# Kernel optimization log

Measured on AMD Instinct MI355X. Metric: run time of the kernel, lower is better.

## Reference

```python
import jax, jax.numpy as jnp
import numpy as np

B, S, H, R = 32, 512, 1024, 64


def _bernoulli(key, shape, p=0.05):
    return (jax.random.uniform(key, shape) < p).astype(jnp.float32)


def setup_inputs() -> dict:
    key = jax.random.key(0)
    ks = jax.random.split(key, 16)
    context = jax.random.normal(ks[0], (B, S, H), dtype=jnp.float32)
    masks = jnp.ones((B, S), dtype=jnp.float32)
    all_subject_heads = _bernoulli(ks[1], (B, S))
    all_subject_tails = _bernoulli(ks[2], (B, S))
    # one-hot subject head/tail positions (tail >= head)
    h_pos = jax.random.randint(ks[3], (B,), 0, S // 2)
    t_pos = h_pos + jax.random.randint(ks[4], (B,), 0, 8)
    subject_head = jax.nn.one_hot(h_pos, S, dtype=jnp.float32)
    subject_tail = jax.nn.one_hot(t_pos, S, dtype=jnp.float32)
    object_heads = _bernoulli(ks[5], (B, S, R))
    object_tails = _bernoulli(ks[6], (B, S, R))
    # learned parameters (PyTorch Linear: y = x @ W.T + b; store as [in, out])
    sc = 1.0 / np.sqrt(H)
    Ws_h = jax.random.uniform(ks[7], (H, 1), minval=-sc, maxval=sc)
    bs_h = jnp.zeros((1,), dtype=jnp.float32)
    Ws_t = jax.random.uniform(ks[8], (H, 1), minval=-sc, maxval=sc)
    bs_t = jnp.zeros((1,), dtype=jnp.float32)
    Wo_h = jax.random.uniform(ks[9], (H, R), minval=-sc, maxval=sc)
    bo_h = jnp.zeros((R,), dtype=jnp.float32)
    Wo_t = jax.random.uniform(ks[10], (H, R), minval=-sc, maxval=sc)
    bo_t = jnp.zeros((R,), dtype=jnp.float32)
    return dict(context=context, masks=masks,
                all_subject_heads=all_subject_heads, all_subject_tails=all_subject_tails,
                subject_head=subject_head, subject_tail=subject_tail,
                object_heads=object_heads, object_tails=object_tails,
                Ws_h=Ws_h, bs_h=bs_h, Ws_t=Ws_t, bs_t=bs_t,
                Wo_h=Wo_h, bo_h=bo_h, Wo_t=Wo_t, bo_t=bo_t)


def _bce_with_logits(logits, targets):
    # numerically stable, matches F.binary_cross_entropy_with_logits(reduction='none')
    return jnp.maximum(logits, 0.0) - logits * targets + jnp.log1p(jnp.exp(-jnp.abs(logits)))


def _masked_loss(gold, pred, mask):
    loss = _bce_with_logits(pred, gold)
    if loss.ndim != mask.ndim:
        mask = mask[..., None]
    return jnp.sum(loss * mask) / jnp.sum(mask)


def reference(context, masks, all_subject_heads, all_subject_tails,
              subject_head, subject_tail, object_heads, object_tails,
              Ws_h, bs_h, Ws_t, bs_t, Wo_h, bo_h, Wo_t, bo_t):
    # subject logits: [B,S]
    pred_subject_heads = (context @ Ws_h + bs_h)[..., 0]
    pred_subject_tails = (context @ Ws_t + bs_t)[..., 0]
    # subject pooling: one-hot [B,S] x context [B,S,H] -> [B,H]
    sub_h = jnp.einsum('bs,bsh->bh', subject_head, context)
    sub_t = jnp.einsum('bs,bsh->bh', subject_tail, context)
    subject = (sub_h + sub_t) * 0.5
    context_subject = context + subject[:, None, :]  # [B,S,H]
    pred_object_heads = context_subject @ Wo_h + bo_h  # [B,S,R]
    pred_object_tails = context_subject @ Wo_t + bo_t  # [B,S,R]
    loss = (_masked_loss(all_subject_heads, pred_subject_heads, masks)
            + _masked_loss(all_subject_tails, pred_subject_tails, masks)
            + _masked_loss(object_heads, pred_object_heads, masks)
            + _masked_loss(object_tails, pred_object_tails, masks))
    return loss
```

## Files before the change

kernel.cpp:

```cpp
#include <hip/hip_runtime.h>


#define B_  32
#define S_  512
#define H_  1024
#define R_  64
#define M_  (B_ * S_)
#define NPAD 160
#define NVALID 130
#define MT 128
#define CGC 80
#define TBLK 20
#define NTHR 512
#define NKS (H_ / 32)

typedef __attribute__((ext_vector_type(4))) float  floatx4;
typedef __attribute__((ext_vector_type(8))) short  short8;
typedef __attribute__((ext_vector_type(8))) unsigned short u16x8;

__device__ __forceinline__ unsigned short f2bf(float f) {
    unsigned int u = __float_as_uint(f);
    u = (u + 0x7FFFu + ((u >> 16) & 1u)) >> 16;
    return (unsigned short)u;
}

__device__ __forceinline__ short8 cvt8(float4 a, float4 b) {
    union { unsigned short us[8]; short8 s8; } u;
    u.us[0] = f2bf(a.x); u.us[1] = f2bf(a.y); u.us[2] = f2bf(a.z); u.us[3] = f2bf(a.w);
    u.us[4] = f2bf(b.x); u.us[5] = f2bf(b.y); u.us[6] = f2bf(b.z); u.us[7] = f2bf(b.w);
    return u.s8;
}

__device__ __forceinline__ void gload16(const void* g, void* l) {
    __builtin_amdgcn_global_load_lds(
        (const __attribute__((address_space(1))) unsigned int*)g,
        (__attribute__((address_space(3))) unsigned int*)l, 16, 0, 0);
}

__global__ __launch_bounds__(256) void aux_kernel(
        const float* __restrict__ ctx, const float* __restrict__ head,
        const float* __restrict__ tail, const float* __restrict__ masks,
        const float* __restrict__ Wo_h, const float* __restrict__ Wo_t,
        const float* __restrict__ Ws_h, const float* __restrict__ Ws_t,
        const float* __restrict__ bo_h, const float* __restrict__ bo_t,
        const float* __restrict__ bs_h, const float* __restrict__ bs_t,
        unsigned short* __restrict__ WtG, float* __restrict__ rowBias,
        float* __restrict__ accum) {
    const int tid = threadIdx.x;
    __shared__ float tr[32][257];
    __shared__ float subj[H_];
    __shared__ float partS[4][256];
    __shared__ int cnt;
    __shared__ int   sidx[8];
    __shared__ float sw[8];

    if (blockIdx.x < TBLK) {
        const int kt = blockIdx.x / 5, nt = blockIdx.x % 5;
        const int k0 = kt * 256, n0 = nt * 32;
        if (n0 < 128) {
            const float* src = (n0 < 64) ? Wo_h : Wo_t;
            const int cb = n0 & 63;
            const int nn = tid & 31, kk = tid >> 5;
#pragma unroll
            for (int i = 0; i < 32; ++i) {
                const int k = k0 + i * 8 + kk;
                tr[nn][i * 8 + kk] = src[(size_t)k * R_ + cb + nn];
            }
            __syncthreads();
#pragma unroll
            for (int p = 0; p < 4; ++p) {
                const int chunk = p * 256 + tid;
                const int n = chunk >> 5;
                const int kc = (chunk & 31) * 8;
                u16x8 v;
#pragma unroll
                for (int j = 0; j < 8; ++j) v[j] = f2bf(tr[n][kc + j]);
                *(u16x8*)(WtG + (size_t)(n0 + n) * H_ + k0 + kc) = v;
            }
        } else {
#pragma unroll
            for (int p = 0; p < 4; ++p) {
                const int chunk = p * 256 + tid;
                const int n = 128 + (chunk >> 5);
                const int kc = (chunk & 31) * 8;
                u16x8 v;
#pragma unroll
                for (int j = 0; j < 8; ++j) {
                    float f = (n == 128) ? Ws_h[k0 + kc + j]
                            : (n == 129) ? Ws_t[k0 + kc + j] : 0.0f;
                    v[j] = f2bf(f);
                }
                *(u16x8*)(WtG + (size_t)n * H_ + k0 + kc) = v;
            }
        }
        return;
    }

    const int b = blockIdx.x - TBLK;
    if (tid == 0) cnt = 0;
    __syncthreads();
    float msk = 0.0f;
    for (int s = tid; s < S_; s += 256) {
        float w = 0.5f * (head[b * S_ + s] + tail[b * S_ + s]);
        if (w != 0.0f) {
            int i = atomicAdd(&cnt, 1);
            if (i < 8) { sidx[i] = s; sw[i] = w; }
        }
        msk += masks[b * S_ + s];
    }
    for (int o = 32; o > 0; o >>= 1) msk += __shfl_down(msk, o, 64);
    if ((tid & 63) == 0) atomicAdd(&accum[1], msk);
    __syncthreads();
    const int nnz = cnt < 8 ? cnt : 8;
    for (int h = tid; h < H_; h += 256) {
        float a = 0.0f;
        for (int i = 0; i < nnz; i++)
            a += sw[i] * ctx[((size_t)b * S_ + sidx[i]) * H_ + h];
        subj[h] = a;
    }
    __syncthreads();
    {
        const int cg = tid & 31;
        const int ks = tid >> 5;
        const int c4 = cg * 4;
        const float* W = (c4 < 64) ? Wo_h : Wo_t;
        const int cc = c4 & 63;
        const int kk0 = ks * 128;
        float ax = 0.f, ay = 0.f, az = 0.f, aw2 = 0.f;
#pragma unroll 4
        for (int k = kk0; k < kk0 + 128; ++k) {
            const float4 w = *(const float4*)(W + (size_t)k * R_ + cc);
            const float sv = subj[k];
            ax += sv * w.x; ay += sv * w.y; az += sv * w.z; aw2 += sv * w.w;
        }
        partS[0][tid] = ax; partS[1][tid] = ay;
        partS[2][tid] = az; partS[3][tid] = aw2;
    }
    __syncthreads();
    if (tid < NPAD) {
        float bias = tid < 64  ? bo_h[tid]
                   : tid < 128 ? bo_t[tid - 64]
                   : tid == 128 ? bs_h[0]
                   : tid == 129 ? bs_t[0] : 0.0f;
        float a2 = 0.0f;
        if (tid < 128) {
            const int g = tid >> 2, j = tid & 3;
#pragma unroll
            for (int s = 0; s < 8; ++s) a2 += partS[j][s * 32 + g];
        }
        rowBias[b * NPAD + tid] = bias + a2;
    }
}

__global__ __launch_bounds__(NTHR) void main_kernel(
        const float* __restrict__ ctx, const unsigned short* __restrict__ WtG,
        const float* __restrict__ rowBias, const float* __restrict__ masks,
        const float* __restrict__ ash, const float* __restrict__ ast,
        const float* __restrict__ oh, const float* __restrict__ ot,
        float* __restrict__ accum, float* __restrict__ accumB,
        float* __restrict__ out) {
    __shared__ __align__(16) unsigned short Bsm[CGC * H_];

    const int tid  = threadIdx.x;
    const int bid  = blockIdx.x;
    const int mb   = bid >> 1, cg = bid & 1;
    const int gm0  = mb * MT;
    const int b    = gm0 >> 9;
    const int wave = tid >> 6, lane = tid & 63;
    const int lr = lane & 15, q = lane >> 4;
    const int col0 = cg * CGC;

#pragma unroll
    for (int p = 0; p < (CGC * H_ * 2 / 16) / NTHR; ++p) {
        const int i = p * NTHR + tid;
        const int row = i >> 7;
        const int bytecol = (i & 127) << 4;
        const int srcb = bytecol ^ ((row & 7) << 4);
        gload16((const char*)(WtG + (size_t)(col0 + row) * H_) + srcb,
                (char*)Bsm + i * 16);
    }
    __syncthreads();

    const int arow = gm0 + wave * 16 + lr;
    const float* aP = ctx + (size_t)arow * H_ + q * 8;
    const int swz = (lr & 7) << 4;
    const int oe = (q << 4) ^ swz;
    const int oo = (64 | (q << 4)) ^ swz;
    int rb5[5];
#pragma unroll
    for (int t = 0; t < 5; ++t) rb5[t] = (t * 16 + lr) * 2048;

    floatx4 acc[5];
#pragma unroll
    for (int t = 0; t < 5; ++t) acc[t] = (floatx4){0.f, 0.f, 0.f, 0.f};

#pragma unroll
    for (int kk = 0; kk < NKS; ++kk) {
        const float4 f0 = *(const float4*)(aP + kk * 32);
        const float4 f1 = *(const float4*)(aP + kk * 32 + 4);
        const short8 afr = cvt8(f0, f1);
        const int kb = (kk >> 1) * 128 + ((kk & 1) ? oo : oe);
#pragma unroll
        for (int t = 0; t < 5; ++t) {
            const short8 bfr = *(const short8*)((const char*)Bsm + rb5[t] + kb);
            acc[t] = __builtin_amdgcn_mfma_f32_16x16x32_bf16(afr, bfr, acc[t], 0, 0, 0);
        }
    }

    float lsum = 0.0f;
#pragma unroll
    for (int t = 0; t < 5; ++t) {
        const int col = col0 + t * 16 + lr;
        if (col < NVALID) {
            const float rbv = rowBias[b * NPAD + col];
#pragma unroll
            for (int i = 0; i < 4; ++i) {
                const int row = gm0 + wave * 16 + q * 4 + i;
                const float l = acc[t][i] + rbv;
                float tgt;
                if (col < 64)        tgt = oh[(size_t)row * R_ + col];
                else if (col < 128)  tgt = ot[(size_t)row * R_ + (col - 64)];
                else if (col == 128) tgt = ash[row];
                else                 tgt = ast[row];
                const float mk = masks[row];
                const float bce = fmaxf(l, 0.0f) - l * tgt + log1pf(__expf(-fabsf(l)));
                lsum += bce * mk;
            }
        }
    }
    for (int o = 32; o > 0; o >>= 1) lsum += __shfl_down(lsum, o, 64);
    if (lane == 0) atomicAdd(&accumB[bid], lsum);
    __syncthreads();
    if (tid == 0) {
        const float s0 = atomicAdd(&accumB[bid], 0.0f);
        atomicAdd(&accum[0], s0);
        __threadfence();
        const unsigned int prev = atomicAdd((unsigned int*)(accum + 2), 1u);
        if (prev == gridDim.x - 1) {
            const float s = atomicAdd(&accum[0], 0.0f);
            const float m = atomicAdd(&accum[1], 0.0f);
            out[0] = s / m;
        }
    }
}

extern "C" void kernel_launch(void* const* d_in, const int* in_sizes, int n_in,
                              void* d_out, int out_size, void* d_ws, size_t ws_size,
                              hipStream_t stream) {
    const float* ctx   = (const float*)d_in[0];
    const float* masks = (const float*)d_in[1];
    const float* ash   = (const float*)d_in[2];
    const float* ast   = (const float*)d_in[3];
    const float* sh    = (const float*)d_in[4];
    const float* st    = (const float*)d_in[5];
    const float* oh    = (const float*)d_in[6];
    const float* ot    = (const float*)d_in[7];
    const float* Ws_h  = (const float*)d_in[8];
    const float* bs_h  = (const float*)d_in[9];
    const float* Ws_t  = (const float*)d_in[10];
    const float* bs_t  = (const float*)d_in[11];
    const float* Wo_h  = (const float*)d_in[12];
    const float* bo_h  = (const float*)d_in[13];
    const float* Wo_t  = (const float*)d_in[14];
    const float* bo_t  = (const float*)d_in[15];
    float* out = (float*)d_out;

    char* ws = (char*)d_ws;
    float* accum   = (float*)(ws + 0);
    float* accumB  = (float*)(ws + 256);
    float* rowBias = (float*)(ws + 2048);
    unsigned short* WtG = (unsigned short*)(ws + 2048 + 32 * NPAD * 4);

    hipMemsetAsync(ws, 0, 1280, stream);
    aux_kernel<<<TBLK + B_, 256, 0, stream>>>(ctx, sh, st, masks, Wo_h, Wo_t,
                                              Ws_h, Ws_t, bo_h, bo_t, bs_h, bs_t,
                                              WtG, rowBias, accum);
    main_kernel<<<(M_ / MT) * 2, NTHR, 0, stream>>>(ctx, WtG, rowBias, masks,
                                                    ash, ast, oh, ot,
                                                    accum, accumB, out);
}
```

Baseline: 177.3 us.

## Compute all output columns per block with K-split LDS staging of weights

Replaces the two column-group blocks per 128-row tile with one 256-thread block per 64-row tile that computes all 144 padded columns. Each block now reads its context rows once instead of twice. The bf16 weight tile is staged into LDS in two 512-wide K phases so it fits in shared memory. The per-block partial sum buffer is removed: each wave atomically adds directly to the global accumulator, and the completion counter is scaled to waves. The trade-off is serialized staging with barriers and no overlap between load and compute, fewer threads per block, and more atomics.

```diff
diff --git a/kernel.cpp b/kernel.cpp
--- a/kernel.cpp
+++ b/kernel.cpp
@@ -8,11 +8,10 @@
 #define M_  (B_ * S_)
 #define NPAD 160
 #define NVALID 130
-#define MT 128
-#define CGC 80
+#define NCOL 144
+#define MT 64
+#define PHK 512
 #define TBLK 20
-#define NTHR 512
-#define NKS (H_ / 32)
 
 typedef __attribute__((ext_vector_type(4))) float  floatx4;
 typedef __attribute__((ext_vector_type(8))) short  short8;
@@ -152,65 +151,71 @@
     }
 }
 
-__global__ __launch_bounds__(NTHR) void main_kernel(
+__global__ __launch_bounds__(256, 1) void main_kernel(
         const float* __restrict__ ctx, const unsigned short* __restrict__ WtG,
         const float* __restrict__ rowBias, const float* __restrict__ masks,
         const float* __restrict__ ash, const float* __restrict__ ast,
         const float* __restrict__ oh, const float* __restrict__ ot,
-        float* __restrict__ accum, float* __restrict__ accumB,
-        float* __restrict__ out) {
-    __shared__ __align__(16) unsigned short Bsm[CGC * H_];
+        float* __restrict__ accum, float* __restrict__ out) {
+    __shared__ __align__(16) unsigned short Bsm[NCOL * PHK];
 
     const int tid  = threadIdx.x;
-    const int bid  = blockIdx.x;
-    const int mb   = bid >> 1, cg = bid & 1;
-    const int gm0  = mb * MT;
+    const int gm0  = blockIdx.x * MT;
     const int b    = gm0 >> 9;
     const int wave = tid >> 6, lane = tid & 63;
     const int lr = lane & 15, q = lane >> 4;
-    const int col0 = cg * CGC;
-
-#pragma unroll
-    for (int p = 0; p < (CGC * H_ * 2 / 16) / NTHR; ++p) {
-        const int i = p * NTHR + tid;
-        const int row = i >> 7;
-        const int bytecol = (i & 127) << 4;
-        const int srcb = bytecol ^ ((row & 7) << 4);
-        gload16((const char*)(WtG + (size_t)(col0 + row) * H_) + srcb,
-                (char*)Bsm + i * 16);
-    }
-    __syncthreads();
-
-    const int arow = gm0 + wave * 16 + lr;
-    const float* aP = ctx + (size_t)arow * H_ + q * 8;
-    const int swz = (lr & 7) << 4;
-    const int oe = (q << 4) ^ swz;
-    const int oo = (64 | (q << 4)) ^ swz;
-    int rb5[5];
-#pragma unroll
-    for (int t = 0; t < 5; ++t) rb5[t] = (t * 16 + lr) * 2048;
-
-    floatx4 acc[5];
-#pragma unroll
-    for (int t = 0; t < 5; ++t) acc[t] = (floatx4){0.f, 0.f, 0.f, 0.f};
-
-#pragma unroll
-    for (int kk = 0; kk < NKS; ++kk) {
-        const float4 f0 = *(const float4*)(aP + kk * 32);
-        const float4 f1 = *(const float4*)(aP + kk * 32 + 4);
-        const short8 afr = cvt8(f0, f1);
-        const int kb = (kk >> 1) * 128 + ((kk & 1) ? oo : oe);
-#pragma unroll
-        for (int t = 0; t < 5; ++t) {
-            const short8 bfr = *(const short8*)((const char*)Bsm + rb5[t] + kb);
-            acc[t] = __builtin_amdgcn_mfma_f32_16x16x32_bf16(afr, bfr, acc[t], 0, 0, 0);
-        }
-    }
+
+#define STAGE(kbase) do {                                                      \
+        _Pragma("unroll")                                                      \
+        for (int p = 0; p < (NCOL * PHK * 2 / 16) / 256; ++p) {        \
+            const int i = p * 256 + tid;                                       \
+            const int row = i >> 6;                                            \
+            const int bcol = (i & 63) << 4;                                    \
+            const int sb = bcol ^ ((row & 7) << 4);                            \
+            gload16((const char*)(WtG + (size_t)row * H_ + (kbase)) + sb,      \
+                    (char*)Bsm + (size_t)i * 16);                              \
+        }                                                                      \
+    } while (0)
+
+    const float* aP = ctx + (size_t)(gm0 + wave * 16 + lr) * H_ + q * 8;
+    const int swzr = (lr & 7) << 4;
+    int rb9[9];
+#pragma unroll
+    for (int t = 0; t < 9; ++t) rb9[t] = (t * 16 + lr) * 1024;
+
+    floatx4 acc[9];
+#pragma unroll
+    for (int t = 0; t < 9; ++t) acc[t] = (floatx4){0.f, 0.f, 0.f, 0.f};
+
+#define COMPUTE(kbase) do {                                                    \
+        _Pragma("unroll")                                                      \
+        for (int ks = 0; ks < PHK / 32; ++ks) {                \
+            const float4 f0 = *(const float4*)(aP + (kbase) + ks * 32);        \
+            const float4 f1 = *(const float4*)(aP + (kbase) + ks * 32 + 4);    \
+            const short8 afr = cvt8(f0, f1);                                   \
+            const int kb = (ks * 64 + q * 16) ^ swzr;                          \
+            _Pragma("unroll")                                                  \
+            for (int t = 0; t < 9; ++t) {                                      \
+                const short8 bfr = *(const short8*)((const char*)Bsm + rb9[t] + kb);\
+                acc[t] = __builtin_amdgcn_mfma_f32_16x16x32_bf16(afr, bfr, acc[t], 0, 0, 0);\
+            }                                                                  \
+        }                                                                      \
+    } while (0)
+
+    STAGE(0);
+    __syncthreads();
+    COMPUTE(0);
+    __syncthreads();
+    STAGE(PHK);
+    __syncthreads();
+    COMPUTE(PHK);
+#undef STAGE
+#undef COMPUTE
 
     float lsum = 0.0f;
 #pragma unroll
-    for (int t = 0; t < 5; ++t) {
-        const int col = col0 + t * 16 + lr;
+    for (int t = 0; t < 9; ++t) {
+        const int col = t * 16 + lr;
         if (col < NVALID) {
             const float rbv = rowBias[b * NPAD + col];
 #pragma unroll
@@ -229,14 +234,11 @@
         }
     }
     for (int o = 32; o > 0; o >>= 1) lsum += __shfl_down(lsum, o, 64);
-    if (lane == 0) atomicAdd(&accumB[bid], lsum);
-    __syncthreads();
-    if (tid == 0) {
-        const float s0 = atomicAdd(&accumB[bid], 0.0f);
-        atomicAdd(&accum[0], s0);
+    if (lane == 0) {
+        atomicAdd(&accum[0], lsum);
         __threadfence();
         const unsigned int prev = atomicAdd((unsigned int*)(accum + 2), 1u);
-        if (prev == gridDim.x - 1) {
+        if (prev == 4u * gridDim.x - 1u) {
             const float s = atomicAdd(&accum[0], 0.0f);
             const float m = atomicAdd(&accum[1], 0.0f);
             out[0] = s / m;
@@ -267,15 +269,13 @@
 
     char* ws = (char*)d_ws;
     float* accum   = (float*)(ws + 0);
-    float* accumB  = (float*)(ws + 256);
-    float* rowBias = (float*)(ws + 2048);
-    unsigned short* WtG = (unsigned short*)(ws + 2048 + 32 * NPAD * 4);
-
-    hipMemsetAsync(ws, 0, 1280, stream);
+    float* rowBias = (float*)(ws + 256);
+    unsigned short* WtG = (unsigned short*)(ws + 256 + 32 * NPAD * 4);
+
+    hipMemsetAsync(accum, 0, 12, stream);
     aux_kernel<<<TBLK + B_, 256, 0, stream>>>(ctx, sh, st, masks, Wo_h, Wo_t,
                                               Ws_h, Ws_t, bo_h, bo_t, bs_h, bs_t,
                                               WtG, rowBias, accum);
-    main_kernel<<<(M_ / MT) * 2, NTHR, 0, stream>>>(ctx, WtG, rowBias, masks,
-                                                    ash, ast, oh, ot,
-                                                    accum, accumB, out);
-}
+    main_kernel<<<M_ / MT, 256, 0, stream>>>(ctx, WtG, rowBias, masks,
+                                             ash, ast, oh, ot, accum, out);
+}
```

Result: slower. 197.5 us (+11.4%).
